# Kernel tuning notes

Measured on AMD Instinct MI355X. Metric: run time of the kernel, lower is better.

## Reference

```python
import jax, jax.numpy as jnp
import numpy as np

NUM_HEADS = 12
HEAD_DIM = 64
HIDDEN = NUM_HEADS * HEAD_DIM
SCALE = 1.0 / float(np.sqrt(HEAD_DIM))


def _split_heads(x):
    # x: [b, d, s, hidden] -> [b, h, d, s, head_dim]  (transpose_for_scores)
    b, d, s, _ = x.shape
    return jnp.transpose(x.reshape(b, d, s, NUM_HEADS, HEAD_DIM), (0, 3, 1, 2, 4))


def _merge_heads(x):
    # [b, h, d, s, e] -> [b, d, s, hidden]  (untranspose_for_scores)
    b, h, d, s, e = x.shape
    return jnp.transpose(x, (0, 2, 3, 1, 4)).reshape(b, d, s, h * e)


def _segment_attention(q, keys, values, masks, num_docs):
    # _cat_forward: broadcast every key/value/mask list entry to num_docs along
    # dim 2, concat along key length, then scaled-dot-product attention.
    b, h = q.shape[0], q.shape[1]
    q = jnp.broadcast_to(q, (b, h, num_docs, q.shape[3], q.shape[4]))
    k = jnp.concatenate([jnp.broadcast_to(t, (b, h, num_docs, t.shape[3], t.shape[4])) for t in keys], axis=3)
    v = jnp.concatenate([jnp.broadcast_to(t, (b, h, num_docs, t.shape[3], t.shape[4])) for t in values], axis=3)
    mask = jnp.concatenate([jnp.broadcast_to(m, (b, 1, num_docs, 1, m.shape[-1])) for m in masks], axis=-1)
    scores = jnp.einsum('bhdqe,bhdke->bhdqk', q, k) * SCALE + mask
    probs = jax.nn.softmax(scores, axis=-1)
    ctx = jnp.einsum('bhdqk,bhdke->bhdqe', probs, v)
    return _merge_heads(ctx)


def setup_inputs() -> dict:
    key = jax.random.key(0)
    ks = jax.random.split(key, 8)
    B, D, Q, S = 2, 16, 32, 512
    inp = {
        'cls': jax.random.normal(ks[0], (B, 1, 1, HIDDEN), jnp.float32),
        'query': jax.random.normal(ks[1], (B, 1, Q, HIDDEN), jnp.float32),
        'doc': jax.random.normal(ks[2], (B, D, S, HIDDEN), jnp.float32),
        'qmask': jnp.zeros((B, 1, 1, 1, Q), jnp.float32),
        'dmask': jnp.zeros((B, 1, D, 1, S), jnp.float32),
        'Wq': jax.random.normal(ks[3], (HIDDEN, HIDDEN), jnp.float32) * 0.02,
        'bq': jnp.zeros((HIDDEN,), jnp.float32),
        'Wk': jax.random.normal(ks[4], (HIDDEN, HIDDEN), jnp.float32) * 0.02,
        'bk': jnp.zeros((HIDDEN,), jnp.float32),
        'Wv': jax.random.normal(ks[5], (HIDDEN, HIDDEN), jnp.float32) * 0.02,
        'bv': jnp.zeros((HIDDEN,), jnp.float32),
    }
    return inp


def reference(cls, query, doc, qmask, dmask, Wq, bq, Wk, bk, Wv, bv):
    num_docs = doc.shape[1]
    b = cls.shape[0]
    # per-segment q/k/v projections + head split
    segs = {}
    for name, hs in (('cls', cls), ('query', query), ('doc', doc)):
        segs[name] = tuple(_split_heads(hs @ W.T + bb) for W, bb in ((Wq, bq), (Wk, bk), (Wv, bv)))
    cmask = jnp.zeros((b, 1, 1, 1, cls.shape[2]), cls.dtype)  # cls token never padded
    masks = {'cls': cmask, 'query': qmask, 'doc': dmask}
    names = ('cls', 'query', 'doc')
    keys = [segs[n][1] for n in names]
    vals = [segs[n][2] for n in names]
    mlist = [masks[n] for n in names]
    # all segment->segment attention flags default True; attention_window_size
    # is None so each segment goes through the _cat_forward path
    outs = [_segment_attention(segs[n][0], keys, vals, mlist, num_docs) for n in names]
    # cls:[b,D,1,H], query:[b,D,Q,H], doc:[b,D,S,H] -> concat along seq for one output
    return jnp.concatenate(outs, axis=2)
```

## Files before the change

### kernel.cpp

```cpp
#include <hip/hip_runtime.h>
#include <hip/hip_bf16.h>

#define NH      12
#define HD      64
#define HID     768
#define B_      2
#define D_      16
#define QL      32
#define SL      512
#define SEQ     545
#define RPB     8225
#define TOT_ROWS 16450
#define PAD_ROWS 16512
#define VT_R    8256
#define WSZ     589824
#define SCALE_  0.125f
#define LOG2E   1.4426950408889634f
#define QSF     0.18033688011112042f

typedef __attribute__((ext_vector_type(8))) short short8;
typedef __attribute__((ext_vector_type(4))) short short4v;
typedef __attribute__((ext_vector_type(4))) float float4v;
typedef __attribute__((ext_vector_type(2))) unsigned int uint2v;

__device__ __forceinline__ short f2bf(float f) {
    __hip_bfloat16 h = __float2bfloat16(f);
    short s; __builtin_memcpy(&s, &h, 2);
    return s;
}

__device__ __forceinline__ unsigned int cvtpk(float a, float b) {
    unsigned int r;
    asm("v_cvt_pk_bf16_f32 %0, %1, %2" : "=v"(r) : "v"(a), "v"(b));
    return r;
}

__device__ __forceinline__ void gl2lds16(const short* g, short* l) {
    __builtin_amdgcn_global_load_lds(
        (const __attribute__((address_space(1))) void*)g,
        (__attribute__((address_space(3))) void*)l, 16, 0, 0);
}

#define PACK_BLKS  12384
#define WPACK_BLKS 1728

__global__ __launch_bounds__(256) void pack_all(
    const float* __restrict__ cls, const float* __restrict__ query,
    const float* __restrict__ doc,
    const float* __restrict__ Wq, const float* __restrict__ Wk,
    const float* __restrict__ Wv,
    short* __restrict__ X, short* __restrict__ Wb)
{
    int bid = blockIdx.x;
    if (bid < PACK_BLKS) {
        int idx = (bid * 256 + threadIdx.x) * 4;
        int row = idx / HID;
        int col = idx - row * HID;
        float4 v = make_float4(0.f, 0.f, 0.f, 0.f);
        if (row < TOT_ROWS) {
            int b = row / RPB;
            int r = row - b * RPB;
            const float* src;
            if (r == 0)        src = cls   + b * HID + col;
            else if (r < 33)   src = query + ((size_t)(b * QL + (r - 1))) * HID + col;
            else               src = doc   + ((size_t)(b * (D_ * SL) + (r - 33))) * HID + col;
            v = *reinterpret_cast<const float4*>(src);
        }
        short4v o;
        o[0] = f2bf(v.x); o[1] = f2bf(v.y); o[2] = f2bf(v.z); o[3] = f2bf(v.w);
        *reinterpret_cast<short4v*>(X + idx) = o;
    } else {
        int idx = ((bid - PACK_BLKS) * 256 + threadIdx.x) * 4;
        int z = idx / WSZ;
        int r = idx - z * WSZ;
        const float* src = (z == 0 ? Wq : (z == 1 ? Wk : Wv)) + r;
        float sc = (z == 0) ? QSF : 1.0f;
        float4 v = *reinterpret_cast<const float4*>(src);
        short4v o;
        o[0] = f2bf(v.x * sc); o[1] = f2bf(v.y * sc);
        o[2] = f2bf(v.z * sc); o[3] = f2bf(v.w * sc);
        *reinterpret_cast<short4v*>(Wb + idx) = o;
    }
}

__global__ __launch_bounds__(256) void proj4u(
    const short* __restrict__ X, const short* __restrict__ Wb,
    const float* __restrict__ bq, const float* __restrict__ bk,
    const float* __restrict__ bv,
    short* __restrict__ Qb, short* __restrict__ Kb, short* __restrict__ Vt)
{
    __shared__ short Xs[2][128 * 32];
    __shared__ short Ws[2][128 * 32];

    int tid = threadIdx.x, lane = tid & 63, wave = tid >> 6;

    int lin = blockIdx.x + 18 * blockIdx.y;
    {
        const int q = 290, r = 2;
        int xcd = lin & 7, seq = lin >> 3;
        lin = (xcd < r ? xcd * (q + 1) : r * (q + 1) + (xcd - r) * q) + seq;
    }
    int mblk = lin / 18;
    int nz   = lin - mblk * 18;
    int zi   = nz % 3;
    int nblk = nz / 3;
    bool vsw = (zi == 2);
    const short* W = Wb + (size_t)zi * WSZ;
    int m0 = mblk * 128, n0 = nblk * 128;

    int moff = (wave & 1) * 64, noff = (wave >> 1) * 64;
    int lr = lane & 15, lg = lane >> 4, lk = lg * 8;
    int srow = lane >> 2, sk = (lane & 3) * 8;

    const short* xg0 = X + (size_t)(m0 + wave * 32 + srow) * HID + sk;
    const short* xg1 = xg0 + (size_t)16 * HID;
    const short* wg0 = W + (size_t)(n0 + wave * 32 + srow) * HID + sk;
    const short* wg1 = wg0 + (size_t)16 * HID;

    float4v acc[4][4];
    for (int mi = 0; mi < 4; ++mi)
        for (int ni = 0; ni < 4; ++ni)
            acc[mi][ni] = (float4v){0.f, 0.f, 0.f, 0.f};

#define PSTAGE(bufi, kt) do {                                   \
    gl2lds16(xg0 + (kt) * 32, &Xs[bufi][wave * 1024]);          \
    gl2lds16(xg1 + (kt) * 32, &Xs[bufi][wave * 1024 + 512]);    \
    gl2lds16(wg0 + (kt) * 32, &Ws[bufi][wave * 1024]);          \
    gl2lds16(wg1 + (kt) * 32, &Ws[bufi][wave * 1024 + 512]); } while (0)

    PSTAGE(0, 0);
#pragma unroll
    for (int kt = 0; kt < 24; ++kt) {
        __syncthreads();
        if (kt < 23) PSTAGE((kt + 1) & 1, kt + 1);
        const short* xb = Xs[kt & 1];
        const short* wb = Ws[kt & 1];
        short8 af[4], bf2[4];
        for (int mi = 0; mi < 4; ++mi)
            af[mi]  = *reinterpret_cast<const short8*>(&xb[(moff + mi * 16 + lr) * 32 + lk]);
        for (int ni = 0; ni < 4; ++ni)
            bf2[ni] = *reinterpret_cast<const short8*>(&wb[(noff + ni * 16 + lr) * 32 + lk]);
        if (!vsw) {
            for (int mi = 0; mi < 4; ++mi)
                for (int ni = 0; ni < 4; ++ni)
                    acc[mi][ni] = __builtin_amdgcn_mfma_f32_16x16x32_bf16(
                        af[mi], bf2[ni], acc[mi][ni], 0, 0, 0);
        } else {
            for (int mi = 0; mi < 4; ++mi)
                for (int ni = 0; ni < 4; ++ni)
                    acc[mi][ni] = __builtin_amdgcn_mfma_f32_16x16x32_bf16(
                        bf2[ni], af[mi], acc[mi][ni], 0, 0, 0);
        }
    }
#undef PSTAGE

    if (!vsw) {
        short* Y = zi == 0 ? Qb : Kb;
        const float* bias = zi == 0 ? bq : bk;
        float bsc = zi == 0 ? QSF : 1.0f;
        for (int ni = 0; ni < 4; ++ni) {
            int gcol = n0 + noff + ni * 16 + lr;
            float bb = bias[gcol] * bsc;
            for (int mi = 0; mi < 4; ++mi) {
                int growb = m0 + moff + mi * 16 + lg * 4;
                for (int r = 0; r < 4; ++r)
                    Y[(size_t)(growb + r) * HID + gcol] = f2bf(acc[mi][ni][r] + bb);
            }
        }
    } else {
        for (int ni = 0; ni < 4; ++ni) {
            float4 b4 = *reinterpret_cast<const float4*>(&bv[n0 + noff + ni * 16 + lg * 4]);
            const float* bbr = reinterpret_cast<const float*>(&b4);
            for (int mi = 0; mi < 4; ++mi) {
                int grow = m0 + moff + mi * 16 + lr;
                if (grow >= TOT_ROWS) continue;
                int b  = grow >= RPB ? 1 : 0;
                int rb = grow - b * RPB;
                int vr = rb < 33 ? rb : rb + 7;
                size_t cb = ((size_t)(b * HID + n0 + noff + ni * 16 + lg * 4)) * VT_R;
                for (int r = 0; r < 4; ++r)
                    Vt[cb + (size_t)r * VT_R + vr] = f2bf(acc[mi][ni][r] + bbr[r]);
            }
        }
    }
}

__device__ __forceinline__ int row_of(int b, int d, int t) {
    t = t > 544 ? 544 : t;
    int base = b * RPB;
    if (t < 512)  return base + 33 + d * SL + t;
    if (t == 512) return base;
    return base + (t - 512);
}

__global__ __launch_bounds__(256) void attn4(
    const short* __restrict__ Qb, const short* __restrict__ Kb,
    const short* __restrict__ Vt,
    const float* __restrict__ qmask, const float* __restrict__ dmask,
    float* __restrict__ out)
{
    __shared__ short Ks[2][64 * 64];
    __shared__ short Vs[2][64 * 64];
    __shared__ float maskv[576];

    int tid  = threadIdx.x;
    int lane = tid & 63, wave = tid >> 6;

    int lin = blockIdx.x + 5 * blockIdx.y;
    {
        int xcd = lin & 7, seq = lin >> 3;
        lin = xcd * 240 + seq;
    }
    int hbd = lin / 5;
    int qc  = lin - hbd * 5;
    int h = hbd >> 5, bd = hbd & 31;
    int b = bd >> 4, d = bd & 15;

    int lr = lane & 15, lg = lane >> 4, lk = lg * 8;
    int base = b * RPB;
    const short* vbase = Vt + (size_t)(b * HID + h * HD) * VT_R;

#define ASTAGE(bufi, kt) do {                                               \
    for (int p = 0; p < 2; ++p) {                                           \
        int s2 = p * 256 + tid;                                             \
        int r = s2 >> 3, c = s2 & 7;                                        \
        const short* g = Kb + (size_t)row_of(b, d, (kt) * 64 + r) * HID     \
                       + h * HD + ((c ^ (r & 7)) * 8);                      \
        gl2lds16(g, &Ks[bufi][(p * 256 + (tid & 0xC0)) * 8]);               \
    }                                                                       \
    for (int p = 0; p < 2; ++p) {                                           \
        int s2 = p * 256 + tid;                                             \
        int rd = s2 >> 3, c = s2 & 7;                                       \
        int tc = (kt) * 64 + ((c ^ (rd & 7)) * 8);                          \
        int vr = tc < 512 ? 40 + d * SL + tc : tc - 512;                    \
        gl2lds16(vbase + (size_t)rd * VT_R + vr,                            \
                 &Vs[bufi][(p * 256 + (tid & 0xC0)) * 8]);                  \
    } } while (0)

    ASTAGE(0, 0);

    for (int i = tid; i < 576; i += 256) {
        float mv;
        if (i < 512)       mv = dmask[(size_t)(b * D_ + d) * SL + i];
        else if (i == 512) mv = 0.f;
        else if (i < 545)  mv = qmask[b * QL + (i - 513)];
        else               mv = -INFINITY;
        maskv[i] = mv * LOG2E;
    }

    short8 bq0[2], bq1[2];
    for (int s = 0; s < 2; ++s) {
        int qtok = qc * 128 + s * 64 + wave * 16 + lr;
        int qrow = qtok < 512 ? base + 33 + d * SL + qtok : base + qtok - 512;
        const short* qp = Qb + (size_t)qrow * HID + h * HD + lk;
        bq0[s] = *reinterpret_cast<const short8*>(qp);
        bq1[s] = *reinterpret_cast<const short8*>(qp + 32);
    }

    float m_i[2] = {-1e30f, -1e30f};
    float lp[2]  = {0.f, 0.f};
    float4v o[2][4];
    for (int s = 0; s < 2; ++s)
        for (int nt = 0; nt < 4; ++nt) o[s][nt] = (float4v){0.f, 0.f, 0.f, 0.f};

#pragma unroll
    for (int kt = 0; kt < 9; ++kt) {
        __syncthreads();
        if (kt < 8) ASTAGE((kt + 1) & 1, kt + 1);
        const short* kb = Ks[kt & 1];
        const short* vbuf = Vs[kt & 1];

        short8 kf0[4], kf1[4];
        for (int nt = 0; nt < 4; ++nt) {
            int r = nt * 16 + lr;
            int x0 = lg ^ (r & 7);
            kf0[nt] = *reinterpret_cast<const short8*>(&kb[r * 64 + x0 * 8]);
            kf1[nt] = *reinterpret_cast<const short8*>(&kb[r * 64 + (x0 ^ 4) * 8]);
        }

        for (int s = 0; s < 2; ++s) {
            float p4[4][4];
            __builtin_amdgcn_s_setprio(1);
            for (int nt = 0; nt < 4; ++nt) {
                float4v z = *reinterpret_cast<const float4v*>(
                    &maskv[kt * 64 + nt * 16 + lg * 4]);
                z = __builtin_amdgcn_mfma_f32_16x16x32_bf16(kf0[nt], bq0[s], z, 0, 0, 0);
                z = __builtin_amdgcn_mfma_f32_16x16x32_bf16(kf1[nt], bq1[s], z, 0, 0, 0);
                for (int r = 0; r < 4; ++r) p4[nt][r] = z[r];
            }
            __builtin_amdgcn_s_setprio(0);

            float c0 = fmaxf(fmaxf(p4[0][0], p4[0][1]), p4[0][2]);
            float c1 = fmaxf(fmaxf(p4[0][3], p4[1][0]), p4[1][1]);
            float c2 = fmaxf(fmaxf(p4[1][2], p4[1][3]), p4[2][0]);
            float c3 = fmaxf(fmaxf(p4[2][1], p4[2][2]), p4[2][3]);
            float c4 = fmaxf(fmaxf(p4[3][0], p4[3][1]), p4[3][2]);
            float lmax = fmaxf(fmaxf(fmaxf(c0, c1), fmaxf(c2, c3)),
                               fmaxf(c4, p4[3][3]));

            if (__any(lmax > m_i[s] + 8.0f)) {
                float tmx = fmaxf(lmax, __shfl_xor(lmax, 16));
                tmx = fmaxf(tmx, __shfl_xor(tmx, 32));
                float mnew = fmaxf(m_i[s], tmx);
                float alpha = exp2f(m_i[s] - mnew);
                m_i[s] = mnew;
                lp[s] *= alpha;
                float al[4];
                for (int r = 0; r < 4; ++r) al[r] = __shfl(alpha, lg * 4 + r);
                for (int nt = 0; nt < 4; ++nt)
                    for (int r = 0; r < 4; ++r) o[s][nt][r] *= al[r];
            }

            for (int nt = 0; nt < 4; ++nt)
                for (int r = 0; r < 4; ++r)
                    p4[nt][r] = exp2f(p4[nt][r] - m_i[s]);
            float s0 = (p4[0][0] + p4[0][1]) + (p4[0][2] + p4[0][3]);
            float s1 = (p4[1][0] + p4[1][1]) + (p4[1][2] + p4[1][3]);
            float s2 = (p4[2][0] + p4[2][1]) + (p4[2][2] + p4[2][3]);
            float s3 = (p4[3][0] + p4[3][1]) + (p4[3][2] + p4[3][3]);
            lp[s] += (s0 + s1) + (s2 + s3);

            unsigned int wa[4], wbv[4];
            for (int nt = 0; nt < 4; ++nt) {
                wa[nt]  = cvtpk(p4[nt][0], p4[nt][1]);
                wbv[nt] = cvtpk(p4[nt][2], p4[nt][3]);
            }
            uint2v tA01 = __builtin_amdgcn_permlane32_swap(wa[0],  wa[1],  false, false);
            uint2v uA01 = __builtin_amdgcn_permlane16_swap(tA01[0], tA01[1], false, false);
            uint2v tB01 = __builtin_amdgcn_permlane32_swap(wbv[0], wbv[1], false, false);
            uint2v uB01 = __builtin_amdgcn_permlane16_swap(tB01[0], tB01[1], false, false);
            uint2v tA23 = __builtin_amdgcn_permlane32_swap(wa[2],  wa[3],  false, false);
            uint2v uA23 = __builtin_amdgcn_permlane16_swap(tA23[0], tA23[1], false, false);
            uint2v tB23 = __builtin_amdgcn_permlane32_swap(wbv[2], wbv[3], false, false);
            uint2v uB23 = __builtin_amdgcn_permlane16_swap(tB23[0], tB23[1], false, false);

            union { unsigned int u[4]; short8 s8; } A0, A1;
            A0.u[0] = uA01[0]; A0.u[1] = uB01[0]; A0.u[2] = uA01[1]; A0.u[3] = uB01[1];
            A1.u[0] = uA23[0]; A1.u[1] = uB23[0]; A1.u[2] = uA23[1]; A1.u[3] = uB23[1];
            short8 ap0 = A0.s8;
            short8 ap1 = A1.s8;

            __builtin_amdgcn_s_setprio(1);
            for (int nt = 0; nt < 4; ++nt) {
                int rd = nt * 16 + lr;
                int x0 = lg ^ (rd & 7);
                short8 bv0 = *reinterpret_cast<const short8*>(&vbuf[rd * 64 + x0 * 8]);
                short8 bv1 = *reinterpret_cast<const short8*>(&vbuf[rd * 64 + (x0 ^ 4) * 8]);
                o[s][nt] = __builtin_amdgcn_mfma_f32_16x16x32_bf16(ap0, bv0, o[s][nt], 0, 0, 0);
                o[s][nt] = __builtin_amdgcn_mfma_f32_16x16x32_bf16(ap1, bv1, o[s][nt], 0, 0, 0);
            }
            __builtin_amdgcn_s_setprio(0);
        }
    }
#undef ASTAGE

    for (int s = 0; s < 2; ++s) {
        float lt = lp[s];
        lt += __shfl_xor(lt, 16);
        lt += __shfl_xor(lt, 32);
        float li[4];
        for (int r = 0; r < 4; ++r) li[r] = __shfl(lt, lg * 4 + r);
        for (int r = 0; r < 4; ++r) {
            int t = qc * 128 + s * 64 + wave * 16 + lg * 4 + r;
            if (t >= SEQ) continue;
            int seq = t < 512 ? 33 + t : (t == 512 ? 0 : t - 512);
            float inv = 1.f / li[r];
            float* op = out + ((size_t)(bd * SEQ + seq)) * HID + h * HD + lr;
            for (int nt = 0; nt < 4; ++nt)
                op[nt * 16] = o[s][nt][r] * inv;
        }
    }
}

extern "C" void kernel_launch(void* const* d_in, const int* in_sizes, int n_in,
                              void* d_out, int out_size, void* d_ws, size_t ws_size,
                              hipStream_t stream)
{
    const float* cls   = (const float*)d_in[0];
    const float* query = (const float*)d_in[1];
    const float* doc   = (const float*)d_in[2];
    const float* qmask = (const float*)d_in[3];
    const float* dmask = (const float*)d_in[4];
    const float* Wq = (const float*)d_in[5];
    const float* bq = (const float*)d_in[6];
    const float* Wk = (const float*)d_in[7];
    const float* bk = (const float*)d_in[8];
    const float* Wv = (const float*)d_in[9];
    const float* bv = (const float*)d_in[10];
    float* out = (float*)d_out;

    short* X  = (short*)d_ws;
    size_t seg = (size_t)PAD_ROWS * HID;
    short* Qb = X + seg;
    short* Kb = Qb + seg;
    short* Vt = Kb + seg;
    short* Wb = (short*)d_out;

    pack_all<<<dim3(PACK_BLKS + WPACK_BLKS), 256, 0, stream>>>(
        cls, query, doc, Wq, Wk, Wv, X, Wb);
    proj4u<<<dim3(18, 129, 1), 256, 0, stream>>>(X, Wb, bq, bk, bv, Qb, Kb, Vt);
    attn4<<<dim3(5, NH * 32, 1), 256, 0, stream>>>(Qb, Kb, Vt, qmask, dmask, out);
}
```

Before: 304.2 us.

## Double projection K-tile to 64 and XOR-swizzle LDS layout

The projection GEMM's K tile grows from 32 to 64, which halves the number of barrier-separated main-loop iterations. An XOR swizzle is applied to the LDS column chunks on both the global-to-LDS copy and the fragment reads, to avoid bank conflicts on the wider rows. The cost is twice the LDS per block, which may lower occupancy, plus more index arithmetic.

```diff
diff --git a/kernel.cpp b/kernel.cpp
--- a/kernel.cpp
+++ b/kernel.cpp
@@ -89,8 +89,8 @@
     const float* __restrict__ bv,
     short* __restrict__ Qb, short* __restrict__ Kb, short* __restrict__ Vt)
 {
-    __shared__ short Xs[2][128 * 32];
-    __shared__ short Ws[2][128 * 32];
+    __shared__ short Xs[2][128 * 64];
+    __shared__ short Ws[2][128 * 64];
 
     int tid = threadIdx.x, lane = tid & 63, wave = tid >> 6;
 
@@ -109,47 +109,69 @@
     int m0 = mblk * 128, n0 = nblk * 128;
 
     int moff = (wave & 1) * 64, noff = (wave >> 1) * 64;
-    int lr = lane & 15, lg = lane >> 4, lk = lg * 8;
-    int srow = lane >> 2, sk = (lane & 3) * 8;
-
-    const short* xg0 = X + (size_t)(m0 + wave * 32 + srow) * HID + sk;
-    const short* xg1 = xg0 + (size_t)16 * HID;
-    const short* wg0 = W + (size_t)(n0 + wave * 32 + srow) * HID + sk;
-    const short* wg1 = wg0 + (size_t)16 * HID;
+    int lr = lane & 15, lg = lane >> 4;
+
+    const short* xsrc[4];
+    const short* wsrc[4];
+#pragma unroll
+    for (int p = 0; p < 4; ++p) {
+        int s = p * 256 + tid;
+        int row = s >> 3, c = s & 7;
+        int col = (c ^ (row & 7)) * 8;
+        xsrc[p] = X + (size_t)(m0 + row) * HID + col;
+        wsrc[p] = W + (size_t)(n0 + row) * HID + col;
+    }
 
     float4v acc[4][4];
     for (int mi = 0; mi < 4; ++mi)
         for (int ni = 0; ni < 4; ++ni)
             acc[mi][ni] = (float4v){0.f, 0.f, 0.f, 0.f};
 
-#define PSTAGE(bufi, kt) do {                                   \
-    gl2lds16(xg0 + (kt) * 32, &Xs[bufi][wave * 1024]);          \
-    gl2lds16(xg1 + (kt) * 32, &Xs[bufi][wave * 1024 + 512]);    \
-    gl2lds16(wg0 + (kt) * 32, &Ws[bufi][wave * 1024]);          \
-    gl2lds16(wg1 + (kt) * 32, &Ws[bufi][wave * 1024 + 512]); } while (0)
+#define PSTAGE(bufi, kt) do {                                               \
+    _Pragma("unroll")                                                       \
+    for (int p = 0; p < 4; ++p) {                                           \
+        gl2lds16(xsrc[p] + (kt) * 64,                                       \
+                 &Xs[bufi][(p * 256 + (tid & 0xC0)) * 8]);                  \
+        gl2lds16(wsrc[p] + (kt) * 64,                                       \
+                 &Ws[bufi][(p * 256 + (tid & 0xC0)) * 8]);                  \
+    } } while (0)
 
     PSTAGE(0, 0);
 #pragma unroll
-    for (int kt = 0; kt < 24; ++kt) {
+    for (int kt = 0; kt < 12; ++kt) {
         __syncthreads();
-        if (kt < 23) PSTAGE((kt + 1) & 1, kt + 1);
+        if (kt < 11) PSTAGE((kt + 1) & 1, kt + 1);
         const short* xb = Xs[kt & 1];
         const short* wb = Ws[kt & 1];
-        short8 af[4], bf2[4];
-        for (int mi = 0; mi < 4; ++mi)
-            af[mi]  = *reinterpret_cast<const short8*>(&xb[(moff + mi * 16 + lr) * 32 + lk]);
-        for (int ni = 0; ni < 4; ++ni)
-            bf2[ni] = *reinterpret_cast<const short8*>(&wb[(noff + ni * 16 + lr) * 32 + lk]);
+        short8 afl[4], afh[4], bfl[4], bfh[4];
+        for (int mi = 0; mi < 4; ++mi) {
+            int r = moff + mi * 16 + lr;
+            int x0 = lg ^ (r & 7);
+            afl[mi] = *reinterpret_cast<const short8*>(&xb[r * 64 + x0 * 8]);
+            afh[mi] = *reinterpret_cast<const short8*>(&xb[r * 64 + (x0 ^ 4) * 8]);
+        }
+        for (int ni = 0; ni < 4; ++ni) {
+            int r = noff + ni * 16 + lr;
+            int x0 = lg ^ (r & 7);
+            bfl[ni] = *reinterpret_cast<const short8*>(&wb[r * 64 + x0 * 8]);
+            bfh[ni] = *reinterpret_cast<const short8*>(&wb[r * 64 + (x0 ^ 4) * 8]);
+        }
         if (!vsw) {
             for (int mi = 0; mi < 4; ++mi)
-                for (int ni = 0; ni < 4; ++ni)
+                for (int ni = 0; ni < 4; ++ni) {
                     acc[mi][ni] = __builtin_amdgcn_mfma_f32_16x16x32_bf16(
-                        af[mi], bf2[ni], acc[mi][ni], 0, 0, 0);
+                        afl[mi], bfl[ni], acc[mi][ni], 0, 0, 0);
+                    acc[mi][ni] = __builtin_amdgcn_mfma_f32_16x16x32_bf16(
+                        afh[mi], bfh[ni], acc[mi][ni], 0, 0, 0);
+                }
         } else {
             for (int mi = 0; mi < 4; ++mi)
-                for (int ni = 0; ni < 4; ++ni)
+                for (int ni = 0; ni < 4; ++ni) {
                     acc[mi][ni] = __builtin_amdgcn_mfma_f32_16x16x32_bf16(
-                        bf2[ni], af[mi], acc[mi][ni], 0, 0, 0);
+                        bfl[ni], afl[mi], acc[mi][ni], 0, 0, 0);
+                    acc[mi][ni] = __builtin_amdgcn_mfma_f32_16x16x32_bf16(
+                        bfh[ni], afh[mi], acc[mi][ni], 0, 0, 0);
+                }
         }
     }
 #undef PSTAGE
```

Measured after the change: 285.4 us. 1.07x faster.
